# Kernel tuning notes

Measured on AMD Instinct MI355X. Metric: run time of the kernel, lower is better.

The kernel has to match this reference:

```python
import jax, jax.numpy as jnp
import numpy as np
import math

B, N, D, O, H = 8, 1024, 512, 512, 8
HD = O // H  # head_dim = 64


def setup_inputs() -> dict:
    key = jax.random.key(0)
    ks = jax.random.split(key, 12)
    x = jax.random.normal(ks[0], (B, N, D), dtype=jnp.float32)
    adj = jax.random.uniform(ks[1], (B, N, N), dtype=jnp.float32)  # unused by forward math
    mask = jax.random.randint(ks[2], (B, N), 0, 2) > 0  # bool padding mask
    # learned params (torch nn.Linear: y = x @ W.T + b)
    qkv_w = jax.random.normal(ks[3], (3 * O, D), dtype=jnp.float32) / math.sqrt(D)
    qkv_b = jnp.zeros((3 * O,), dtype=jnp.float32)
    # self_loop_W: 1/head_dim + U(0,1), per head, non-trainable
    self_loop_W = (1.0 / HD + jax.random.uniform(ks[4], (1, H, 1, 1))).astype(jnp.float32)
    w1 = jax.random.normal(ks[5], (O, O), dtype=jnp.float32) / math.sqrt(O)
    b1 = jnp.zeros((O,), dtype=jnp.float32)
    w2 = jax.random.normal(ks[6], (O, O), dtype=jnp.float32) / math.sqrt(O)
    b2 = jnp.zeros((O,), dtype=jnp.float32)
    wr = jax.random.normal(ks[7], (O, D), dtype=jnp.float32) / math.sqrt(D)
    br = jnp.zeros((O,), dtype=jnp.float32)
    return {"x": x, "adj": adj, "mask": mask, "self_loop_W": self_loop_W,
            "qkv_w": qkv_w, "qkv_b": qkv_b, "w1": w1, "b1": b1,
            "w2": w2, "b2": b2, "wr": wr, "br": br}


def reference(x, adj, mask, self_loop_W, qkv_w, qkv_b, w1, b1, w2, b2, wr, br):
    fmask = mask.astype(x.dtype)  # [B,N]
    # --- MoireAttention ---
    qkv = x @ qkv_w.T + qkv_b                       # [B,N,3O]
    qkv = qkv.reshape(B, N, 3, H, HD).transpose(2, 0, 3, 1, 4)  # [3,B,H,N,hd]
    Q, K, V = qkv[0], qkv[1], qkv[2]
    scores = jnp.einsum('bhnd,bhmd->bhnm', Q, K) / math.sqrt(HD)  # [B,H,N,N]
    eye = jnp.eye(N, dtype=scores.dtype)
    scores = scores + eye[None, None] * self_loop_W  # per-head diagonal self-loop bias
    mask2d = mask[:, None, :, None] & mask[:, None, None, :]  # [B,1,N,N]
    scores = jnp.where(mask2d, scores, jnp.asarray(-1e6, scores.dtype))
    attn = jax.nn.softmax(scores, axis=-1)
    h = jnp.einsum('bhnm,bhmd->bhnd', attn, V)      # [B,H,N,hd]
    h = h.transpose(0, 2, 1, 3).reshape(B, N, O)
    # --- mask, FFN (eval mode: noise/dropout are identity), mask ---
    h = h * fmask[..., None]
    h = jax.nn.relu(h @ w1.T + b1) @ w2.T + b2
    h = h * fmask[..., None]
    # --- residual blend ---
    x_proj = x @ wr.T + br
    return h * 0.5 + x_proj * 0.5
```

## Files before the change

### kernel.cpp

```cpp
#include <hip/hip_runtime.h>
#include <hip/hip_bf16.h>

typedef __attribute__((ext_vector_type(8))) short short8;
typedef __attribute__((ext_vector_type(4))) float f32x4;
typedef __attribute__((ext_vector_type(4))) short short4v;

#define BB 8
#define NN 1024
#define DD 512
#define OO 512
#define HH 8
#define HD 64
#define MM (BB * NN)

#define QSC 0.18033688f
#define KSHIFT -11.54156032f
#define KMASKED -30000.0f

__device__ __forceinline__ void gload_lds16(const void* g, void* l) {
  __builtin_amdgcn_global_load_lds(
      (const __attribute__((address_space(1))) void*)g,
      (__attribute__((address_space(3))) void*)l, 16, 0, 0);
}

__device__ __forceinline__ uint2 cvt4(float4 v) {
  union { uint2 u; __hip_bfloat16 h[4]; } t;
  t.h[0] = __float2bfloat16(v.x);
  t.h[1] = __float2bfloat16(v.y);
  t.h[2] = __float2bfloat16(v.z);
  t.h[3] = __float2bfloat16(v.w);
  return t.u;
}

#define SEG_N 10
struct ConvArgs {
  const float* src[SEG_N];
  __hip_bfloat16* dst[SEG_N];
  int n4[SEG_N];
};

__global__ void convert_kernel(ConvArgs a) {
  const int t = blockIdx.y;
  const int n4 = a.n4[t];
  const float4* fs = (const float4*)a.src[t];
  uint2* d = (uint2*)a.dst[t];
  for (int i = blockIdx.x * blockDim.x + threadIdx.x; i < n4;
       i += gridDim.x * blockDim.x)
    d[i] = cvt4(fs[i]);
}

__global__ __launch_bounds__(256) void gemm_qkv(
    const __hip_bfloat16* __restrict__ A0, const __hip_bfloat16* __restrict__ B0,
    const __hip_bfloat16* __restrict__ bias0,
    __hip_bfloat16* __restrict__ out0, __hip_bfloat16* __restrict__ out1,
    __hip_bfloat16* __restrict__ out2, int Kd) {
  __shared__ __align__(16) __hip_bfloat16 smem[8192];
  __hip_bfloat16* As = smem;
  __hip_bfloat16* Bs = smem + 4096;

  const int tid  = threadIdx.x;
  const int wave = tid >> 6;
  const int lane = tid & 63;
  const int fl   = lane & 15;
  const int fk   = (lane >> 4) * 8;
  const int wm   = (wave & 1) * 64;
  const int wn   = (wave >> 1) * 64;
  const int bid     = blockIdx.x;
  const int rowpart = 8 * (bid & 7) + ((bid >> 3) & 7);
  const int colpart = bid >> 6;
  const int m0 = rowpart * 128;
  const int n0 = colpart * 128;
  const int glr  = lane >> 2;
  const int glc  = (lane & 3) * 8;

  f32x4 acc[4][4];
#pragma unroll
  for (int i = 0; i < 4; ++i)
#pragma unroll
    for (int j = 0; j < 4; ++j) acc[i][j] = (f32x4){0.f, 0.f, 0.f, 0.f};

  char* lb = (char*)smem;
  for (int k0 = 0; k0 < Kd; k0 += 32) {
    __syncthreads();
    gload_lds16(A0 + (size_t)(m0 + wave * 16 + glr) * Kd + k0 + glc,
                lb + wave * 1024 + lane * 16);
    gload_lds16(A0 + (size_t)(m0 + 64 + wave * 16 + glr) * Kd + k0 + glc,
                lb + (wave + 4) * 1024 + lane * 16);
    gload_lds16(B0 + (size_t)(n0 + wave * 16 + glr) * Kd + k0 + glc,
                lb + 8192 + wave * 1024 + lane * 16);
    gload_lds16(B0 + (size_t)(n0 + 64 + wave * 16 + glr) * Kd + k0 + glc,
                lb + 8192 + (wave + 4) * 1024 + lane * 16);
    __syncthreads();

    short8 af[4], bfr[4];
#pragma unroll
    for (int i = 0; i < 4; ++i)
      af[i] = *(const short8*)&As[(wm + i * 16 + fl) * 32 + fk];
#pragma unroll
    for (int j = 0; j < 4; ++j)
      bfr[j] = *(const short8*)&Bs[(wn + j * 16 + fl) * 32 + fk];
#pragma unroll
    for (int i = 0; i < 4; ++i)
#pragma unroll
      for (int j = 0; j < 4; ++j)
        acc[i][j] = __builtin_amdgcn_mfma_f32_16x16x32_bf16(af[i], bfr[j],
                                                            acc[i][j], 0, 0, 0);
  }

  const int rb = (lane >> 4) * 4;
  const int part = n0 >> 9;
  if (part < 2) {
    __hip_bfloat16* dst = (part == 0) ? out0 : out1;
    const float scf = (part == 0) ? QSC : 1.0f;
#pragma unroll
    for (int j = 0; j < 4; ++j) {
      const int colb  = n0 + wn + j * 16;
      const int o     = colb & 511;
      const int headq = o >> 6;
      const int d     = (o & 63) + fl;
      const float bi  = __bfloat162float(bias0[colb + fl]);
#pragma unroll
      for (int i = 0; i < 4; ++i) {
#pragma unroll
        for (int r = 0; r < 4; ++r) {
          const int row = m0 + wm + i * 16 + rb + r;
          const int bb  = row >> 10;
          const int nn  = row & 1023;
          dst[((size_t)((bb << 3) + headq) * NN + nn) * HD + d] =
              __float2bfloat16((acc[i][j][r] + bi) * scf);
        }
      }
    }
  } else {
    __syncthreads();
    __hip_bfloat16* tsc = smem + wave * 1120;
    const int bb  = (m0 + wm) >> 10;
    const int nnb = (m0 + wm) & 1023;
    const int dl  = lane >> 2;
    const int cc  = (lane & 3) * 16;
#pragma unroll
    for (int j = 0; j < 4; ++j) {
      const int colb  = n0 + wn + j * 16;
      const int o     = colb & 511;
      const int headq = o >> 6;
      const int dbase = o & 63;
      const float bi  = __bfloat162float(bias0[colb + fl]);
#pragma unroll
      for (int i = 0; i < 4; ++i) {
#pragma unroll
        for (int r = 0; r < 4; ++r) {
          const int rr = i * 16 + rb + r;
          tsc[fl * 70 + rr] = __float2bfloat16(acc[i][j][r] + bi);
        }
      }
      uint4 r0 = *(const uint4*)&tsc[dl * 70 + cc];
      uint4 r1 = *(const uint4*)&tsc[dl * 70 + cc + 8];
      __hip_bfloat16* vdst =
          out2 + ((size_t)((bb << 3) + headq) * HD + dbase + dl) * NN + nnb;
      *(uint4*)&vdst[cc] = r0;
      *(uint4*)&vdst[cc + 8] = r1;
    }
  }
}

template <int MODE>
__global__ __launch_bounds__(256) void gemm64(
    const __hip_bfloat16* __restrict__ A0, const __hip_bfloat16* __restrict__ B0,
    const __hip_bfloat16* __restrict__ A1, const __hip_bfloat16* __restrict__ B1,
    const __hip_bfloat16* __restrict__ bias0, const __hip_bfloat16* __restrict__ bias1,
    const int* __restrict__ mask,
    __hip_bfloat16* __restrict__ out0, float* __restrict__ outf,
    int N, int Kd) {
  __shared__ __align__(16) __hip_bfloat16 smem[4096];
  __hip_bfloat16* As = smem;
  __hip_bfloat16* Bs = smem + 2048;

  const int tid  = threadIdx.x;
  const int wave = tid >> 6;
  const int lane = tid & 63;
  const int fl   = lane & 15;
  const int fk   = (lane >> 4) * 8;
  const int wm   = (wave & 1) * 32;
  const int wn   = (wave >> 1) * 32;
  const int bid     = blockIdx.x;
  const int rowpart = 16 * (bid & 7) + ((bid >> 3) & 15);
  const int colpart = bid >> 7;
  const int m0 = rowpart * 64;
  const int n0 = colpart * 64;
  const int glr  = lane >> 2;
  const int glc  = (lane & 3) * 8;

  f32x4 acc[2][2];
#pragma unroll
  for (int i = 0; i < 2; ++i)
#pragma unroll
    for (int j = 0; j < 2; ++j) acc[i][j] = (f32x4){0.f, 0.f, 0.f, 0.f};

  char* lb = (char*)smem;
  const int npairs = (MODE == 2) ? 2 : 1;
  for (int p = 0; p < npairs; ++p) {
    const __hip_bfloat16* Ap = (p == 0) ? A0 : A1;
    const __hip_bfloat16* Bp = (p == 0) ? B0 : B1;
    for (int k0 = 0; k0 < Kd; k0 += 32) {
      __syncthreads();
      gload_lds16(Ap + (size_t)(m0 + wave * 16 + glr) * Kd + k0 + glc,
                  lb + wave * 1024 + lane * 16);
      gload_lds16(Bp + (size_t)(n0 + wave * 16 + glr) * Kd + k0 + glc,
                  lb + 4096 + wave * 1024 + lane * 16);
      __syncthreads();

      short8 af[2], bfr[2];
#pragma unroll
      for (int i = 0; i < 2; ++i)
        af[i] = *(const short8*)&As[(wm + i * 16 + fl) * 32 + fk];
#pragma unroll
      for (int j = 0; j < 2; ++j)
        bfr[j] = *(const short8*)&Bs[(wn + j * 16 + fl) * 32 + fk];
#pragma unroll
      for (int i = 0; i < 2; ++i)
#pragma unroll
        for (int j = 0; j < 2; ++j)
          acc[i][j] = __builtin_amdgcn_mfma_f32_16x16x32_bf16(af[i], bfr[j],
                                                              acc[i][j], 0, 0, 0);
    }
  }

  const int rb = (lane >> 4) * 4;
  if (MODE == 1) {
#pragma unroll
    for (int j = 0; j < 2; ++j) {
      const int col  = n0 + wn + j * 16 + fl;
      const float bi = __bfloat162float(bias0[col]);
#pragma unroll
      for (int i = 0; i < 2; ++i) {
#pragma unroll
        for (int r = 0; r < 4; ++r) {
          const int row = m0 + wm + i * 16 + rb + r;
          float v = fmaxf(acc[i][j][r] + bi, 0.f);
          if (mask[row] == 0) v = 0.f;
          out0[(size_t)row * N + col] = __float2bfloat16(v);
        }
      }
    }
  } else {
#pragma unroll
    for (int j = 0; j < 2; ++j) {
      const int col   = n0 + wn + j * 16 + fl;
      const float b2v = __bfloat162float(bias0[col]);
      const float brv = __bfloat162float(bias1[col]);
#pragma unroll
      for (int i = 0; i < 2; ++i) {
#pragma unroll
        for (int r = 0; r < 4; ++r) {
          const int row = m0 + wm + i * 16 + rb + r;
          const float v = acc[i][j][r] + brv + (mask[row] != 0 ? b2v : 0.f);
          outf[(size_t)row * N + col] = 0.5f * v;
        }
      }
    }
  }
}

__global__ __launch_bounds__(512) void attn_kernel(
    const __hip_bfloat16* __restrict__ Qb, const __hip_bfloat16* __restrict__ Kb,
    const __hip_bfloat16* __restrict__ Vt, const __hip_bfloat16* __restrict__ slw,
    const int* __restrict__ mask, __hip_bfloat16* __restrict__ hb) {
  __shared__ __hip_bfloat16 Qs[128 * 72];
  __shared__ __hip_bfloat16 Ks[64 * 72];
  __shared__ __hip_bfloat16 Vs[64 * 72];
  __shared__ __hip_bfloat16 Ps[128 * 72];
  __shared__ float Msf[NN];

  const int tid  = threadIdx.x;
  const int wave = tid >> 6;
  const int lane = tid & 63;
  const int fl   = lane & 15;
  const int quad = lane >> 4;
  const int fk   = quad * 8;
  const int rb   = quad * 4;
  const int bh   = blockIdx.x & 63;
  const int qblk = blockIdx.x >> 6;
  const int b    = bh >> 3;
  const int head = bh & 7;
  const int q0   = qblk * 128;

  const float slwL2 = __bfloat162float(slw[head]) * 1.44269504f;

  {
    const int srow = tid >> 2;
    const int sc   = (tid & 3) * 16;
    const __hip_bfloat16* qg = Qb + ((size_t)bh * NN + q0) * HD;
    uint4 v0 = *(const uint4*)(qg + srow * HD + sc);
    uint4 v1 = *(const uint4*)(qg + srow * HD + sc + 8);
    *(uint4*)&Qs[srow * 72 + sc] = v0;
    *(uint4*)&Qs[srow * 72 + sc + 8] = v1;
#pragma unroll
    for (int k = 0; k < 2; ++k) {
      const int idx = tid * 2 + k;
      Msf[idx] = (mask[b * NN + idx] != 0) ? KSHIFT : KMASKED;
    }
  }
  __syncthreads();
  const short8 qa0 = *(const short8*)&Qs[(wave * 16 + fl) * 72 + fk];
  const short8 qa1 = *(const short8*)&Qs[(wave * 16 + fl) * 72 + fk + 32];

  const int srow2 = tid >> 3;
  const int sc2   = (tid & 7) * 8;

  float lsum = 0.f;
  f32x4 Oacc[4];
#pragma unroll
  for (int t = 0; t < 4; ++t) Oacc[t] = (f32x4){0.f, 0.f, 0.f, 0.f};

  const int kbdiag = 2 * qblk + (wave >> 2);

  for (int kb = 0; kb < NN / 64; ++kb) {
    const int kbase = kb * 64;
    __syncthreads();
    {
      const __hip_bfloat16* kg = Kb + ((size_t)bh * NN + kbase) * HD;
      uint4 v0 = *(const uint4*)(kg + srow2 * HD + sc2);
      *(uint4*)&Ks[srow2 * 72 + sc2] = v0;
      const __hip_bfloat16* vg = Vt + ((size_t)bh * HD + srow2) * NN + kbase;
      uint4 w0 = *(const uint4*)(vg + sc2);
      *(uint4*)&Vs[srow2 * 72 + sc2] = w0;
    }
    __syncthreads();

    f32x4 sfr[4];
#pragma unroll
    for (int j = 0; j < 4; ++j) {
      const short8 kf0 = *(const short8*)&Ks[(j * 16 + fl) * 72 + fk];
      const short8 kf1 = *(const short8*)&Ks[(j * 16 + fl) * 72 + fk + 32];
      f32x4 z = (f32x4){0.f, 0.f, 0.f, 0.f};
      z = __builtin_amdgcn_mfma_f32_16x16x32_bf16(kf0, qa0, z, 0, 0, 0);
      z = __builtin_amdgcn_mfma_f32_16x16x32_bf16(kf1, qa1, z, 0, 0, 0);
      sfr[j] = z;
    }

    if (kb == kbdiag) {
      if ((fl >> 2) == quad) sfr[wave & 3][fl & 3] += slwL2;
    }

#pragma unroll
    for (int j = 0; j < 4; ++j) {
      const f32x4 mb4 = *(const f32x4*)&Msf[kbase + j * 16 + quad * 4];
      union { short4v s; __hip_bfloat16 h[4]; } pu;
      float ps = 0.f;
#pragma unroll
      for (int e = 0; e < 4; ++e) {
        const float pv = exp2f(sfr[j][e] + mb4[e]);
        ps += pv;
        pu.h[e] = __float2bfloat16(pv);
      }
      lsum += ps;
      *(short4v*)&Ps[(wave * 16 + fl) * 72 + j * 16 + quad * 4] = pu.s;
    }

    const short8 pa0 = *(const short8*)&Ps[(wave * 16 + fl) * 72 + fk];
    const short8 pa1 = *(const short8*)&Ps[(wave * 16 + fl) * 72 + fk + 32];
#pragma unroll
    for (int t = 0; t < 4; ++t) {
      const short8 vf0 = *(const short8*)&Vs[(t * 16 + fl) * 72 + fk];
      const short8 vf1 = *(const short8*)&Vs[(t * 16 + fl) * 72 + fk + 32];
      Oacc[t] = __builtin_amdgcn_mfma_f32_16x16x32_bf16(pa0, vf0, Oacc[t], 0, 0, 0);
      Oacc[t] = __builtin_amdgcn_mfma_f32_16x16x32_bf16(pa1, vf1, Oacc[t], 0, 0, 0);
    }
  }

  float l = lsum;
  l += __shfl_xor(l, 16, 64);
  l += __shfl_xor(l, 32, 64);
  const int qrow_me = q0 + wave * 16 + fl;
  const float qm = (mask[b * NN + qrow_me] != 0) ? 1.f : 0.f;
  const float sf = qm / fmaxf(l, 1e-30f);

  float scl[4];
#pragma unroll
  for (int r = 0; r < 4; ++r) scl[r] = __shfl(sf, rb + r, 64);

#pragma unroll
  for (int t = 0; t < 4; ++t) {
    const int d = t * 16 + fl;
#pragma unroll
    for (int r = 0; r < 4; ++r) {
      const int qrow_g = q0 + wave * 16 + rb + r;
      hb[(size_t)(b * NN + qrow_g) * OO + head * HD + d] =
          __float2bfloat16(Oacc[t][r] * scl[r]);
    }
  }
}

extern "C" void kernel_launch(void* const* d_in, const int* in_sizes, int n_in,
                              void* d_out, int out_size, void* d_ws, size_t ws_size,
                              hipStream_t stream) {
  const float* x_raw    = (const float*)d_in[0];
  const int* mask       = (const int*)d_in[2];
  const float* slw_raw  = (const float*)d_in[3];
  const float* qkvw_raw = (const float*)d_in[4];
  const float* qkvb_raw = (const float*)d_in[5];
  const float* w1_raw   = (const float*)d_in[6];
  const float* b1_raw   = (const float*)d_in[7];
  const float* w2_raw   = (const float*)d_in[8];
  const float* b2_raw   = (const float*)d_in[9];
  const float* wr_raw   = (const float*)d_in[10];
  const float* br_raw   = (const float*)d_in[11];
  float* outf           = (float*)d_out;

  __hip_bfloat16* p = (__hip_bfloat16*)d_ws;
  __hip_bfloat16* xc    = p; p += (size_t)MM * DD;
  __hip_bfloat16* qkvwc = p; p += 3 * OO * DD;
  __hip_bfloat16* w1c   = p; p += OO * OO;
  __hip_bfloat16* w2c   = p; p += OO * OO;
  __hip_bfloat16* wrc   = p; p += OO * DD;
  __hip_bfloat16* qkvbc = p; p += 3 * OO;
  __hip_bfloat16* b1c   = p; p += OO;
  __hip_bfloat16* b2c   = p; p += OO;
  __hip_bfloat16* brc   = p; p += OO;
  __hip_bfloat16* slwc  = p; p += 64;
  const size_t ebuf = (size_t)BB * HH * NN * HD;
  __hip_bfloat16* Qb = p; p += ebuf;
  __hip_bfloat16* Kb = p; p += ebuf;
  __hip_bfloat16* Vb = p; p += ebuf;
  __hip_bfloat16* hb = (__hip_bfloat16*)d_out;
  __hip_bfloat16* tb = Kb;

  if (ws_size < (size_t)((char*)p - (char*)d_ws)) return;

  ConvArgs ca;
  ca.src[0] = x_raw;    ca.dst[0] = xc;    ca.n4[0] = MM * DD / 4;
  ca.src[1] = qkvw_raw; ca.dst[1] = qkvwc; ca.n4[1] = 3 * OO * DD / 4;
  ca.src[2] = w1_raw;   ca.dst[2] = w1c;   ca.n4[2] = OO * OO / 4;
  ca.src[3] = w2_raw;   ca.dst[3] = w2c;   ca.n4[3] = OO * OO / 4;
  ca.src[4] = wr_raw;   ca.dst[4] = wrc;   ca.n4[4] = OO * DD / 4;
  ca.src[5] = qkvb_raw; ca.dst[5] = qkvbc; ca.n4[5] = 3 * OO / 4;
  ca.src[6] = b1_raw;   ca.dst[6] = b1c;   ca.n4[6] = OO / 4;
  ca.src[7] = b2_raw;   ca.dst[7] = b2c;   ca.n4[7] = OO / 4;
  ca.src[8] = br_raw;   ca.dst[8] = brc;   ca.n4[8] = OO / 4;
  ca.src[9] = slw_raw;  ca.dst[9] = slwc;  ca.n4[9] = HH / 4;
  convert_kernel<<<dim3(128, SEG_N), 256, 0, stream>>>(ca);

  gemm_qkv<<<768, 256, 0, stream>>>(xc, qkvwc, qkvbc, Qb, Kb, Vb, DD);
  attn_kernel<<<BB * HH * (NN / 128), 512, 0, stream>>>(Qb, Kb, Vb, slwc, mask, hb);
  gemm64<1><<<1024, 256, 0, stream>>>(
      hb, w1c, nullptr, nullptr, b1c, nullptr, mask, tb, nullptr, OO, OO);
  gemm64<2><<<1024, 256, 0, stream>>>(
      tb, w2c, xc, wrc, b2c, brc, mask, nullptr, outf, OO, DD);
}
```

Before: 220.1 us.

## Widen FFN GEMM tiles and prefetch 128-key blocks in attention

The FFN GEMMs now use 64x128 output tiles (four B fragments per wave, a third LDS load) and launch half as many blocks. This raises reuse of the A tile and cuts block count. The attention kernel now processes 128-key blocks with register prefetch of the next K/V tile, so global loads overlap compute. It also reuses the Q buffer for P, adds s_setprio around the MFMA sections, and rewrites the diagonal self-loop bias for the new block size. The tradeoffs are higher register pressure and LDS use, and with 512 GEMM blocks some CUs may sit idle.

```diff
diff --git a/kernel.cpp b/kernel.cpp
--- a/kernel.cpp
+++ b/kernel.cpp
@@ -164,14 +164,14 @@
 }
 
 template <int MODE>
-__global__ __launch_bounds__(256) void gemm64(
+__global__ __launch_bounds__(256) void gemm_ffn(
     const __hip_bfloat16* __restrict__ A0, const __hip_bfloat16* __restrict__ B0,
     const __hip_bfloat16* __restrict__ A1, const __hip_bfloat16* __restrict__ B1,
     const __hip_bfloat16* __restrict__ bias0, const __hip_bfloat16* __restrict__ bias1,
     const int* __restrict__ mask,
     __hip_bfloat16* __restrict__ out0, float* __restrict__ outf,
     int N, int Kd) {
-  __shared__ __align__(16) __hip_bfloat16 smem[4096];
+  __shared__ __align__(16) __hip_bfloat16 smem[6144];
   __hip_bfloat16* As = smem;
   __hip_bfloat16* Bs = smem + 2048;
 
@@ -181,20 +181,20 @@
   const int fl   = lane & 15;
   const int fk   = (lane >> 4) * 8;
   const int wm   = (wave & 1) * 32;
-  const int wn   = (wave >> 1) * 32;
+  const int wn   = (wave >> 1) * 64;
   const int bid     = blockIdx.x;
   const int rowpart = 16 * (bid & 7) + ((bid >> 3) & 15);
   const int colpart = bid >> 7;
   const int m0 = rowpart * 64;
-  const int n0 = colpart * 64;
+  const int n0 = colpart * 128;
   const int glr  = lane >> 2;
   const int glc  = (lane & 3) * 8;
 
-  f32x4 acc[2][2];
+  f32x4 acc[2][4];
 #pragma unroll
   for (int i = 0; i < 2; ++i)
 #pragma unroll
-    for (int j = 0; j < 2; ++j) acc[i][j] = (f32x4){0.f, 0.f, 0.f, 0.f};
+    for (int j = 0; j < 4; ++j) acc[i][j] = (f32x4){0.f, 0.f, 0.f, 0.f};
 
   char* lb = (char*)smem;
   const int npairs = (MODE == 2) ? 2 : 1;
@@ -207,19 +207,21 @@
                   lb + wave * 1024 + lane * 16);
       gload_lds16(Bp + (size_t)(n0 + wave * 16 + glr) * Kd + k0 + glc,
                   lb + 4096 + wave * 1024 + lane * 16);
+      gload_lds16(Bp + (size_t)(n0 + 64 + wave * 16 + glr) * Kd + k0 + glc,
+                  lb + 8192 + wave * 1024 + lane * 16);
       __syncthreads();
 
-      short8 af[2], bfr[2];
+      short8 af[2], bfr[4];
 #pragma unroll
       for (int i = 0; i < 2; ++i)
         af[i] = *(const short8*)&As[(wm + i * 16 + fl) * 32 + fk];
 #pragma unroll
-      for (int j = 0; j < 2; ++j)
+      for (int j = 0; j < 4; ++j)
         bfr[j] = *(const short8*)&Bs[(wn + j * 16 + fl) * 32 + fk];
 #pragma unroll
       for (int i = 0; i < 2; ++i)
 #pragma unroll
-        for (int j = 0; j < 2; ++j)
+        for (int j = 0; j < 4; ++j)
           acc[i][j] = __builtin_amdgcn_mfma_f32_16x16x32_bf16(af[i], bfr[j],
                                                               acc[i][j], 0, 0, 0);
     }
@@ -228,7 +230,7 @@
   const int rb = (lane >> 4) * 4;
   if (MODE == 1) {
 #pragma unroll
-    for (int j = 0; j < 2; ++j) {
+    for (int j = 0; j < 4; ++j) {
       const int col  = n0 + wn + j * 16 + fl;
       const float bi = __bfloat162float(bias0[col]);
 #pragma unroll
@@ -244,7 +246,7 @@
     }
   } else {
 #pragma unroll
-    for (int j = 0; j < 2; ++j) {
+    for (int j = 0; j < 4; ++j) {
       const int col   = n0 + wn + j * 16 + fl;
       const float b2v = __bfloat162float(bias0[col]);
       const float brv = __bfloat162float(bias1[col]);
@@ -265,10 +267,9 @@
     const __hip_bfloat16* __restrict__ Qb, const __hip_bfloat16* __restrict__ Kb,
     const __hip_bfloat16* __restrict__ Vt, const __hip_bfloat16* __restrict__ slw,
     const int* __restrict__ mask, __hip_bfloat16* __restrict__ hb) {
-  __shared__ __hip_bfloat16 Qs[128 * 72];
-  __shared__ __hip_bfloat16 Ks[64 * 72];
-  __shared__ __hip_bfloat16 Vs[64 * 72];
-  __shared__ __hip_bfloat16 Ps[128 * 72];
+  __shared__ __align__(16) __hip_bfloat16 QPs[128 * 72];
+  __shared__ __align__(16) __hip_bfloat16 Ks[128 * 72];
+  __shared__ __align__(16) __hip_bfloat16 Vs[64 * 136];
   __shared__ float Msf[NN];
 
   const int tid  = threadIdx.x;
@@ -292,8 +293,8 @@
     const __hip_bfloat16* qg = Qb + ((size_t)bh * NN + q0) * HD;
     uint4 v0 = *(const uint4*)(qg + srow * HD + sc);
     uint4 v1 = *(const uint4*)(qg + srow * HD + sc + 8);
-    *(uint4*)&Qs[srow * 72 + sc] = v0;
-    *(uint4*)&Qs[srow * 72 + sc + 8] = v1;
+    *(uint4*)&QPs[srow * 72 + sc] = v0;
+    *(uint4*)&QPs[srow * 72 + sc + 8] = v1;
 #pragma unroll
     for (int k = 0; k < 2; ++k) {
       const int idx = tid * 2 + k;
@@ -301,35 +302,47 @@
     }
   }
   __syncthreads();
-  const short8 qa0 = *(const short8*)&Qs[(wave * 16 + fl) * 72 + fk];
-  const short8 qa1 = *(const short8*)&Qs[(wave * 16 + fl) * 72 + fk + 32];
-
-  const int srow2 = tid >> 3;
-  const int sc2   = (tid & 7) * 8;
+  const short8 qa0 = *(const short8*)&QPs[(wave * 16 + fl) * 72 + fk];
+  const short8 qa1 = *(const short8*)&QPs[(wave * 16 + fl) * 72 + fk + 32];
+
+  const int srK = tid >> 2;
+  const int scK = (tid & 3) * 16;
+  const int srV = tid >> 3;
+  const int scV = (tid & 7) * 16;
+
+  const __hip_bfloat16* kgb = Kb + (size_t)bh * NN * HD;
+  const __hip_bfloat16* vgb = Vt + (size_t)bh * HD * NN;
+
+  uint4 kr0 = *(const uint4*)(kgb + (size_t)srK * HD + scK);
+  uint4 kr1 = *(const uint4*)(kgb + (size_t)srK * HD + scK + 8);
+  uint4 vr0 = *(const uint4*)(vgb + (size_t)srV * NN + scV);
+  uint4 vr1 = *(const uint4*)(vgb + (size_t)srV * NN + scV + 8);
 
   float lsum = 0.f;
   f32x4 Oacc[4];
 #pragma unroll
   for (int t = 0; t < 4; ++t) Oacc[t] = (f32x4){0.f, 0.f, 0.f, 0.f};
 
-  const int kbdiag = 2 * qblk + (wave >> 2);
-
-  for (int kb = 0; kb < NN / 64; ++kb) {
-    const int kbase = kb * 64;
+  for (int kb = 0; kb < NN / 128; ++kb) {
     __syncthreads();
-    {
-      const __hip_bfloat16* kg = Kb + ((size_t)bh * NN + kbase) * HD;
-      uint4 v0 = *(const uint4*)(kg + srow2 * HD + sc2);
-      *(uint4*)&Ks[srow2 * 72 + sc2] = v0;
-      const __hip_bfloat16* vg = Vt + ((size_t)bh * HD + srow2) * NN + kbase;
-      uint4 w0 = *(const uint4*)(vg + sc2);
-      *(uint4*)&Vs[srow2 * 72 + sc2] = w0;
-    }
+    *(uint4*)&Ks[srK * 72 + scK] = kr0;
+    *(uint4*)&Ks[srK * 72 + scK + 8] = kr1;
+    *(uint4*)&Vs[srV * 136 + scV] = vr0;
+    *(uint4*)&Vs[srV * 136 + scV + 8] = vr1;
     __syncthreads();
 
-    f32x4 sfr[4];
-#pragma unroll
-    for (int j = 0; j < 4; ++j) {
+    if (kb + 1 < NN / 128) {
+      const int nk = (kb + 1) * 128;
+      kr0 = *(const uint4*)(kgb + (size_t)(nk + srK) * HD + scK);
+      kr1 = *(const uint4*)(kgb + (size_t)(nk + srK) * HD + scK + 8);
+      vr0 = *(const uint4*)(vgb + (size_t)srV * NN + nk + scV);
+      vr1 = *(const uint4*)(vgb + (size_t)srV * NN + nk + scV + 8);
+    }
+
+    f32x4 sfr[8];
+    __builtin_amdgcn_s_setprio(1);
+#pragma unroll
+    for (int j = 0; j < 8; ++j) {
       const short8 kf0 = *(const short8*)&Ks[(j * 16 + fl) * 72 + fk];
       const short8 kf1 = *(const short8*)&Ks[(j * 16 + fl) * 72 + fk + 32];
       f32x4 z = (f32x4){0.f, 0.f, 0.f, 0.f};
@@ -337,34 +350,48 @@
       z = __builtin_amdgcn_mfma_f32_16x16x32_bf16(kf1, qa1, z, 0, 0, 0);
       sfr[j] = z;
     }
-
-    if (kb == kbdiag) {
-      if ((fl >> 2) == quad) sfr[wave & 3][fl & 3] += slwL2;
-    }
-
-#pragma unroll
-    for (int j = 0; j < 4; ++j) {
-      const f32x4 mb4 = *(const f32x4*)&Msf[kbase + j * 16 + quad * 4];
-      union { short4v s; __hip_bfloat16 h[4]; } pu;
-      float ps = 0.f;
-#pragma unroll
-      for (int e = 0; e < 4; ++e) {
-        const float pv = exp2f(sfr[j][e] + mb4[e]);
-        ps += pv;
-        pu.h[e] = __float2bfloat16(pv);
-      }
-      lsum += ps;
-      *(short4v*)&Ps[(wave * 16 + fl) * 72 + j * 16 + quad * 4] = pu.s;
-    }
-
-    const short8 pa0 = *(const short8*)&Ps[(wave * 16 + fl) * 72 + fk];
-    const short8 pa1 = *(const short8*)&Ps[(wave * 16 + fl) * 72 + fk + 32];
-#pragma unroll
-    for (int t = 0; t < 4; ++t) {
-      const short8 vf0 = *(const short8*)&Vs[(t * 16 + fl) * 72 + fk];
-      const short8 vf1 = *(const short8*)&Vs[(t * 16 + fl) * 72 + fk + 32];
-      Oacc[t] = __builtin_amdgcn_mfma_f32_16x16x32_bf16(pa0, vf0, Oacc[t], 0, 0, 0);
-      Oacc[t] = __builtin_amdgcn_mfma_f32_16x16x32_bf16(pa1, vf1, Oacc[t], 0, 0, 0);
+    __builtin_amdgcn_s_setprio(0);
+
+    if (kb == qblk && (fl >> 2) == quad) {
+#pragma unroll
+      for (int j = 0; j < 8; ++j)
+        if (wave == j) {
+#pragma unroll
+          for (int e = 0; e < 4; ++e)
+            if ((fl & 3) == e) sfr[j][e] += slwL2;
+        }
+    }
+
+    const int kbase = kb * 128;
+#pragma unroll
+    for (int c = 0; c < 2; ++c) {
+#pragma unroll
+      for (int jj = 0; jj < 4; ++jj) {
+        const f32x4 s4  = sfr[c * 4 + jj];
+        const f32x4 mb4 = *(const f32x4*)&Msf[kbase + c * 64 + jj * 16 + quad * 4];
+        union { short4v s; __hip_bfloat16 h[4]; } pu;
+        float ps = 0.f;
+#pragma unroll
+        for (int e = 0; e < 4; ++e) {
+          const float pv = exp2f(s4[e] + mb4[e]);
+          ps += pv;
+          pu.h[e] = __float2bfloat16(pv);
+        }
+        lsum += ps;
+        *(short4v*)&QPs[(wave * 16 + fl) * 72 + jj * 16 + quad * 4] = pu.s;
+      }
+
+      const short8 pa0 = *(const short8*)&QPs[(wave * 16 + fl) * 72 + fk];
+      const short8 pa1 = *(const short8*)&QPs[(wave * 16 + fl) * 72 + fk + 32];
+      __builtin_amdgcn_s_setprio(1);
+#pragma unroll
+      for (int t = 0; t < 4; ++t) {
+        const short8 vf0 = *(const short8*)&Vs[(t * 16 + fl) * 136 + c * 64 + fk];
+        const short8 vf1 = *(const short8*)&Vs[(t * 16 + fl) * 136 + c * 64 + fk + 32];
+        Oacc[t] = __builtin_amdgcn_mfma_f32_16x16x32_bf16(pa0, vf0, Oacc[t], 0, 0, 0);
+        Oacc[t] = __builtin_amdgcn_mfma_f32_16x16x32_bf16(pa1, vf1, Oacc[t], 0, 0, 0);
+      }
+      __builtin_amdgcn_s_setprio(0);
     }
   }
 
@@ -442,8 +469,8 @@
 
   gemm_qkv<<<768, 256, 0, stream>>>(xc, qkvwc, qkvbc, Qb, Kb, Vb, DD);
   attn_kernel<<<BB * HH * (NN / 128), 512, 0, stream>>>(Qb, Kb, Vb, slwc, mask, hb);
-  gemm64<1><<<1024, 256, 0, stream>>>(
+  gemm_ffn<1><<<512, 256, 0, stream>>>(
       hb, w1c, nullptr, nullptr, b1c, nullptr, mask, tb, nullptr, OO, OO);
-  gemm64<2><<<1024, 256, 0, stream>>>(
+  gemm_ffn<2><<<512, 256, 0, stream>>>(
       tb, w2c, xc, wrc, b2c, brc, mask, nullptr, outf, OO, DD);
 }
```

Result: slower. 237.6 us (+7.9%).
